# Optimization experiments

Hardware: AMD Instinct MI355X
Metric: run time of the kernel (lower is better)

Reference implementation:

```python
import jax, jax.numpy as jnp
import numpy as np

B, S, D, H = 4, 2048, 1024, 16
DK = D // H

def setup_inputs() -> dict:
    key = jax.random.key(0)
    ks = jax.random.split(key, 11)
    scale = 1.0 / np.sqrt(D)
    inp = {
        'q': jax.random.normal(ks[0], (B, S, D), jnp.float32),
        'k': jax.random.normal(ks[1], (B, S, D), jnp.float32),
        'v': jax.random.normal(ks[2], (B, S, D), jnp.float32),
        'Wq': jax.random.normal(ks[3], (D, D), jnp.float32) * scale,
        'bq': jnp.zeros((D,), jnp.float32),
        'Wk': jax.random.normal(ks[4], (D, D), jnp.float32) * scale,
        'bk': jnp.zeros((D,), jnp.float32),
        'Wv': jax.random.normal(ks[5], (D, D), jnp.float32) * scale,
        'bv': jnp.zeros((D,), jnp.float32),
        'Wo': jax.random.normal(ks[6], (D, D), jnp.float32) * scale,
        'bo': jnp.zeros((D,), jnp.float32),
        # diagonal mask: 0 on the diagonal (self position masked out), 1 elsewhere
        'mask': (1 - jnp.eye(S, dtype=jnp.int32))[None, None, :, :],
    }
    return inp


def reference(q, k, v, Wq, bq, Wk, bk, Wv, bv, Wo, bo, mask):
    def proj(x, W, b):
        # [B,S,D] -> [B,H,S,DK]
        y = x @ W.T + b
        return y.reshape(B, S, H, DK).transpose(0, 2, 1, 3)

    qh = proj(q, Wq, bq)
    kh = proj(k, Wk, bk)
    vh = proj(v, Wv, bv)

    scores = jnp.einsum('bhsd,bhtd->bhst', qh, kh) / jnp.sqrt(jnp.float32(DK))
    scores = jnp.where(mask == 0, jnp.finfo(scores.dtype).min, scores)
    attn = jax.nn.softmax(scores, axis=-1)  # dropout is identity in eval mode
    out = jnp.einsum('bhst,bhtd->bhsd', attn, vh)
    out = out.transpose(0, 2, 1, 3).reshape(B, S, D)
    return out @ Wo.T + bo
```

## Files before the change

kernel.cpp:

```cpp
#include <hip/hip_runtime.h>
#include <stdint.h>

#define S_LEN 2048
#define D_DIM 1024
#define NB 4
#define NH 16
#define DKH 64
#define M_ROWS (NB * S_LEN)
#define PLD 72

typedef float  f32x4 __attribute__((ext_vector_type(4)));
typedef short  s16x8 __attribute__((ext_vector_type(8)));
typedef unsigned short u16;
typedef u16    u16x4 __attribute__((ext_vector_type(4)));

#define AS1 __attribute__((address_space(1)))
#define AS3 __attribute__((address_space(3)))

__device__ __forceinline__ void gload16(const u16* g, u16* l) {
    __builtin_amdgcn_global_load_lds((const AS1 void*)g, (AS3 void*)l, 16, 0, 0);
}

__device__ __forceinline__ u16 f2bf(float f) {
    uint32_t u = __builtin_bit_cast(uint32_t, f);
    return (u16)((u + 0x7fffu + ((u >> 16) & 1u)) >> 16);
}
__device__ __forceinline__ u16 f2bf_cheap(float f) {
    uint32_t u = __builtin_bit_cast(uint32_t, f);
    return (u16)((u + 0x8000u) >> 16);
}

__global__ __launch_bounds__(256) void conv_kernel(const float* __restrict__ src,
                                                   u16* __restrict__ dst, int n)
{
    int i = (blockIdx.x * 256 + threadIdx.x) * 8;
    if (i + 8 > n) return;
    f32x4 a = *(const f32x4*)(src + i);
    f32x4 b = *(const f32x4*)(src + i + 4);
    s16x8 r;
#pragma unroll
    for (int j = 0; j < 4; ++j) r[j]     = (short)f2bf(a[j]);
#pragma unroll
    for (int j = 0; j < 4; ++j) r[j + 4] = (short)f2bf(b[j]);
    *(s16x8*)(dst + i) = r;
}

__global__ __launch_bounds__(256) void conv3w_kernel(const float* __restrict__ a,
                                                     const float* __restrict__ b,
                                                     const float* __restrict__ c,
                                                     u16* __restrict__ dst)
{
    const int z = blockIdx.z;
    const float* src = (z == 0) ? a : (z == 1) ? b : c;
    int i = (blockIdx.x * 256 + threadIdx.x) * 8;
    f32x4 lo = *(const f32x4*)(src + i);
    f32x4 hi = *(const f32x4*)(src + i + 4);
    s16x8 r;
#pragma unroll
    for (int j = 0; j < 4; ++j) r[j]     = (short)f2bf(lo[j]);
#pragma unroll
    for (int j = 0; j < 4; ++j) r[j + 4] = (short)f2bf(hi[j]);
    *(s16x8*)(dst + (size_t)z * (D_DIM * D_DIM) + i) = r;
}

__global__ __launch_bounds__(256) void conv3x_kernel(const float* __restrict__ a,
                                                     const float* __restrict__ b,
                                                     const float* __restrict__ c,
                                                     u16* __restrict__ da,
                                                     u16* __restrict__ db,
                                                     u16* __restrict__ dc)
{
    const int z = blockIdx.z;
    const float* src = (z == 0) ? a : (z == 1) ? b : c;
    u16* dst         = (z == 0) ? da : (z == 1) ? db : dc;
    int i = (blockIdx.x * 256 + threadIdx.x) * 8;
    f32x4 lo = *(const f32x4*)(src + i);
    f32x4 hi = *(const f32x4*)(src + i + 4);
    s16x8 r;
#pragma unroll
    for (int j = 0; j < 4; ++j) r[j]     = (short)f2bf(lo[j]);
#pragma unroll
    for (int j = 0; j < 4; ++j) r[j + 4] = (short)f2bf(hi[j]);
    *(s16x8*)(dst + i) = r;
}

__device__ __forceinline__ void stage64(const u16* __restrict__ X,
                                        const u16* __restrict__ Wt,
                                        int m0, int n0, int k0,
                                        u16* As, u16* Bs, int tid, int wv)
{
#pragma unroll
    for (int i = 0; i < 2; ++i) {
        const int c   = tid + i * 256;
        const int row = c >> 3;
        const int sg  = (c & 7) ^ (row & 7);
        gload16(&X[(size_t)(m0 + row) * D_DIM + k0 + sg * 8],
                &As[(i * 256 + wv * 64) * 8]);
    }
#pragma unroll
    for (int i = 0; i < 4; ++i) {
        const int c   = tid + i * 256;
        const int row = c >> 3;
        const int sg  = (c & 7) ^ (row & 7);
        gload16(&Wt[(size_t)(n0 + row) * D_DIM + k0 + sg * 8],
                &Bs[(i * 256 + wv * 64) * 8]);
    }
}

__device__ __forceinline__ void compute64(const u16* As, const u16* Bs,
                                          f32x4 acc[2][4],
                                          int wm, int wn, int ln, int quad, int l7)
{
#pragma unroll
    for (int ks = 0; ks < 2; ++ks) {
        const int sA = ((ks * 4 + quad) ^ l7) * 8;
        s16x8 af[2], bfr[4];
#pragma unroll
        for (int t = 0; t < 2; ++t)
            af[t]  = *(const s16x8*)&As[(wm * 32 + t * 16 + ln) * 64 + sA];
#pragma unroll
        for (int t = 0; t < 4; ++t)
            bfr[t] = *(const s16x8*)&Bs[(wn * 64 + t * 16 + ln) * 64 + sA];
#pragma unroll
        for (int tM = 0; tM < 2; ++tM)
#pragma unroll
            for (int tN = 0; tN < 4; ++tN)
                acc[tM][tN] = __builtin_amdgcn_mfma_f32_16x16x32_bf16(
                    af[tM], bfr[tN], acc[tM][tN], 0, 0, 0);
    }
}

__device__ __forceinline__ void gemm64_body(const u16* __restrict__ X,
                                            const u16* __restrict__ Wt,
                                            int m0, int n0,
                                            u16* As, u16* Bs,
                                            f32x4 acc[2][4])
{
    const int tid  = threadIdx.x;
    const int wv   = tid >> 6;
    const int lane = tid & 63;
    const int ln   = lane & 15;
    const int quad = lane >> 4;
    const int wm   = wv >> 1;
    const int wn   = wv & 1;
    const int l7   = ln & 7;

    for (int k0 = 0; k0 < D_DIM; k0 += 64) {
        __syncthreads();
        stage64(X, Wt, m0, n0, k0, As, Bs, tid, wv);
        __syncthreads();
        compute64(As, Bs, acc, wm, wn, ln, quad, l7);
    }
}

__global__ __launch_bounds__(256) void proj64_kernel(
    const u16* __restrict__ xq, const u16* __restrict__ xk,
    const u16* __restrict__ xv, const u16* __restrict__ Wb,
    const float* __restrict__ bq, const float* __restrict__ bk,
    const float* __restrict__ bv,
    u16* __restrict__ Qh, u16* __restrict__ Kh, u16* __restrict__ Vt,
    int mode0)
{
    __shared__ __attribute__((aligned(16))) u16 As[64 * 64];
    __shared__ __attribute__((aligned(16))) u16 Bs[128 * 64];

    const int mode = mode0 + blockIdx.z;
    const u16* X      = (mode == 0) ? xq : (mode == 1) ? xk : xv;
    const u16* Wt     = Wb + (size_t)mode * (D_DIM * D_DIM);
    const float* bias = (mode == 0) ? bq : (mode == 1) ? bk : bv;
    const float qscale = (mode == 0) ? 0.18033688011112042f : 1.0f;

    const int lin = blockIdx.y * 8 + blockIdx.x;
    const int n0  = (lin & 7) * 128;
    const int m0  = (lin >> 3) * 64;

    f32x4 zero = {0.f, 0.f, 0.f, 0.f};
    f32x4 acc[2][4];
#pragma unroll
    for (int i = 0; i < 2; ++i)
#pragma unroll
        for (int j = 0; j < 4; ++j) acc[i][j] = zero;

    gemm64_body(X, Wt, m0, n0, As, Bs, acc);

    const int tid  = threadIdx.x;
    const int wv   = tid >> 6;
    const int lane = tid & 63;
    const int ln   = lane & 15;
    const int quad = lane >> 4;
    const int wm   = wv >> 1;
    const int wn   = wv & 1;

#pragma unroll
    for (int tM = 0; tM < 2; ++tM) {
#pragma unroll
        for (int tN = 0; tN < 4; ++tN) {
            const int ng = n0 + wn * 64 + tN * 16 + ln;
            const float bf32 = bias[ng];
            const int h  = ng >> 6;
            const int dk = ng & 63;
            const int mbase = m0 + wm * 32 + tM * 16 + quad * 4;
            const int b = mbase >> 11;
            const int s = mbase & 2047;
            if (mode == 2) {
                u16x4 pk;
#pragma unroll
                for (int r = 0; r < 4; ++r) pk[r] = f2bf(acc[tM][tN][r] + bf32);
                *(u16x4*)&Vt[((size_t)((b * NH + h) * DKH + dk)) * S_LEN + s] = pk;
            } else {
                u16* dst = (mode == 0) ? Qh : Kh;
#pragma unroll
                for (int r = 0; r < 4; ++r)
                    dst[((size_t)(b * NH + h) * S_LEN + (s + r)) * DKH + dk] =
                        f2bf((acc[tM][tN][r] + bf32) * qscale);
            }
        }
    }
}

__global__ __launch_bounds__(256) void attn_kernel(
    const u16* __restrict__ Qh, const u16* __restrict__ Kh,
    const u16* __restrict__ Vt, u16* __restrict__ ctx)
{
    __shared__ __attribute__((aligned(16))) u16 Ks[64 * 64];
    __shared__ __attribute__((aligned(16))) u16 Vs[64 * 64];
    __shared__ __attribute__((aligned(16))) u16 QPs[64 * PLD];

    const int tid  = threadIdx.x;
    const int wv   = tid >> 6;
    const int lane = tid & 63;
    const int ln   = lane & 15;
    const int quad = lane >> 4;
    const int l7   = ln & 7;

    const int lin = blockIdx.y * 32 + blockIdx.x;
    const int xcd = lin & 7;
    const int t_  = lin >> 3;
    const int bh  = xcd * 8 + (t_ >> 5);
    const int q0  = (t_ & 31) * 64;

    const size_t qkbase = (size_t)bh * S_LEN * DKH;
    const size_t vbase  = (size_t)bh * DKH * S_LEN;

#pragma unroll
    for (int i = 0; i < 2; ++i) {
        const int c = tid + i * 256, row = c >> 3;
        const int sg = (c & 7) ^ (row & 7);
        gload16(&Qh[qkbase + (size_t)(q0 + row) * DKH + sg * 8],
                &QPs[(i * 256 + wv * 64) * 8]);
    }
    __syncthreads();

    s16x8 aq[2];
#pragma unroll
    for (int ks = 0; ks < 2; ++ks)
        aq[ks] = *(const s16x8*)&QPs[(wv * 16 + ln) * 64 + (((ks * 4 + quad) ^ l7) * 8)];

    float l_part[4] = {0.f, 0.f, 0.f, 0.f};
    f32x4 zero = {0.f, 0.f, 0.f, 0.f};
    f32x4 o_acc[4] = {zero, zero, zero, zero};

    const int rbase = q0 + wv * 16 + quad * 4;
    const int rowA = wv * 16 + ln;
    const int rotA = (((rowA >> 2) & 7)) * 8;
    const int rotW = ((4 * wv + quad) & 7) * 8;

    for (int kb = 0; kb < S_LEN; kb += 64) {
        __syncthreads();
#pragma unroll
        for (int i = 0; i < 2; ++i) {
            const int c = tid + i * 256, row = c >> 3;
            const int sg = (c & 7) ^ (row & 7);
            const int lb = (i * 256 + wv * 64) * 8;
            gload16(&Kh[qkbase + (size_t)(kb + row) * DKH + sg * 8], &Ks[lb]);
            gload16(&Vt[vbase + (size_t)row * S_LEN + kb + sg * 8], &Vs[lb]);
        }
        __syncthreads();

        f32x4 sf[4];
#pragma unroll
        for (int nt = 0; nt < 4; ++nt) {
            f32x4 acc = zero;
#pragma unroll
            for (int ks = 0; ks < 2; ++ks) {
                s16x8 bk_ = *(const s16x8*)&Ks[(nt * 16 + ln) * 64 + (((ks * 4 + quad) ^ l7) * 8)];
                acc = __builtin_amdgcn_mfma_f32_16x16x32_bf16(aq[ks], bk_, acc, 0, 0, 0);
            }
            sf[nt] = acc;
        }

        if (kb == q0) {
#pragma unroll
            for (int nt = 0; nt < 4; ++nt)
#pragma unroll
                for (int r = 0; r < 4; ++r) {
                    float p = __builtin_amdgcn_exp2f(sf[nt][r]);
                    if (rbase + r == kb + nt * 16 + ln) p = 0.f;
                    sf[nt][r] = p;
                    l_part[r] += p;
                }
        } else {
#pragma unroll
            for (int nt = 0; nt < 4; ++nt)
#pragma unroll
                for (int r = 0; r < 4; ++r) {
                    float p = __builtin_amdgcn_exp2f(sf[nt][r]);
                    sf[nt][r] = p;
                    l_part[r] += p;
                }
        }

#pragma unroll
        for (int nt = 0; nt < 4; ++nt)
#pragma unroll
            for (int r = 0; r < 4; ++r) {
                int row  = wv * 16 + quad * 4 + r;
                int col  = ((nt * 16 + ln) + rotW) & 63;
                QPs[row * PLD + col] = f2bf_cheap(sf[nt][r]);
            }

#pragma unroll
        for (int ks = 0; ks < 2; ++ks) {
            int colA = ((ks * 32 + quad * 8) + rotA) & 63;
            s16x8 ap = *(const s16x8*)&QPs[rowA * PLD + colA];
#pragma unroll
            for (int nt = 0; nt < 4; ++nt) {
                s16x8 bvv = *(const s16x8*)&Vs[(nt * 16 + ln) * 64 + (((ks * 4 + quad) ^ l7) * 8)];
                o_acc[nt] = __builtin_amdgcn_mfma_f32_16x16x32_bf16(ap, bvv, o_acc[nt], 0, 0, 0);
            }
        }
    }

#pragma unroll
    for (int r = 0; r < 4; ++r) {
#pragma unroll
        for (int off = 1; off < 16; off <<= 1)
            l_part[r] += __shfl_xor(l_part[r], off, 16);
    }

    const int b = bh >> 4;
    const int h = bh & 15;
#pragma unroll
    for (int nt = 0; nt < 4; ++nt) {
#pragma unroll
        for (int r = 0; r < 4; ++r) {
            float val = o_acc[nt][r] / l_part[r];
            int sg = q0 + wv * 16 + quad * 4 + r;
            ctx[((size_t)b * S_LEN + sg) * D_DIM + h * DKH + nt * 16 + ln] = f2bf(val);
        }
    }
}

__global__ __launch_bounds__(256) void oproj64_kernel(
    const u16* __restrict__ ctx, const u16* __restrict__ WoB,
    const float* __restrict__ bo, float* __restrict__ out, float sentinel)
{
    __shared__ __attribute__((aligned(16))) u16 As[64 * 64];
    __shared__ __attribute__((aligned(16))) u16 Bs[128 * 64];

    const int lin = blockIdx.y * 8 + blockIdx.x;
    const int n0  = (lin & 7) * 128;
    const int m0  = (lin >> 3) * 64;

    f32x4 zero = {0.f, 0.f, 0.f, 0.f};
    f32x4 acc[2][4];
#pragma unroll
    for (int i = 0; i < 2; ++i)
#pragma unroll
        for (int j = 0; j < 4; ++j) acc[i][j] = zero;

    gemm64_body(ctx, WoB, m0, n0, As, Bs, acc);

    const int tid  = threadIdx.x;
    const int wv   = tid >> 6;
    const int lane = tid & 63;
    const int ln   = lane & 15;
    const int quad = lane >> 4;
    const int wm   = wv >> 1;
    const int wn   = wv & 1;

#pragma unroll
    for (int tM = 0; tM < 2; ++tM) {
#pragma unroll
        for (int tN = 0; tN < 4; ++tN) {
            const int ng = n0 + wn * 64 + tN * 16 + ln;
            const float bf32 = bo[ng];
            const int mbase = m0 + wm * 32 + tM * 16 + quad * 4;
#pragma unroll
            for (int r = 0; r < 4; ++r) {
                float val = acc[tM][tN][r] + bf32;
                if (mbase + r == 0 && ng == 0) val += sentinel;
                out[(size_t)(mbase + r) * D_DIM + ng] = val;
            }
        }
    }
}

extern "C" void kernel_launch(void* const* d_in, const int* in_sizes, int n_in,
                              void* d_out, int out_size, void* d_ws, size_t ws_size,
                              hipStream_t stream)
{
    const float* q  = (const float*)d_in[0];
    const float* k  = (const float*)d_in[1];
    const float* v  = (const float*)d_in[2];
    const float* Wq = (const float*)d_in[3];
    const float* bq = (const float*)d_in[4];
    const float* Wk = (const float*)d_in[5];
    const float* bk = (const float*)d_in[6];
    const float* Wv = (const float*)d_in[7];
    const float* bv = (const float*)d_in[8];
    const float* Wo = (const float*)d_in[9];
    const float* bo = (const float*)d_in[10];

    const size_t headSz = (size_t)NB * NH * S_LEN * DKH;
    const int    WN     = D_DIM * D_DIM;
    u16* Qh  = (u16*)d_ws;
    u16* Kh  = Qh + headSz;
    u16* Vt  = Kh + headSz;
    u16* ctx = Vt + headSz;
    u16* Wb  = (u16*)d_out;
    u16* xk  = Wb + 3 * WN;
    u16* xv  = Qh;
    u16* xq  = ctx;
    u16* WoB = Qh;
    float* out = (float*)d_out;

    float sentinel = 0.f;
    {
        const int expect[12] = {8388608, 8388608, 8388608, 1048576, 1024, 1048576,
                                1024, 1048576, 1024, 1048576, 1024, 4194304};
        bool ok = (n_in == 12);
        for (int i = 0; ok && i < 12; ++i) ok = (in_sizes[i] == expect[i]);
        if (!ok)                               sentinel = 1000.f;
        else if (ws_size < 4 * headSz * 2)     sentinel = 2000.f;
        else if (out_size != (int)headSz)      sentinel = 3000.f;
    }

    conv3w_kernel<<<dim3(WN / 2048, 1, 3), 256, 0, stream>>>(Wq, Wk, Wv, Wb);
    conv3x_kernel<<<dim3((int)(headSz / 2048), 1, 3), 256, 0, stream>>>(
        v, q, k, xv, xq, xk);

    proj64_kernel<<<dim3(8, M_ROWS / 64, 1), 256, 0, stream>>>(
        xq, xk, xv, Wb, bq, bk, bv, Qh, Kh, Vt, 2);
    proj64_kernel<<<dim3(8, M_ROWS / 64, 2), 256, 0, stream>>>(
        xq, xk, xv, Wb, bq, bk, bv, Qh, Kh, Vt, 0);

    attn_kernel<<<dim3(32, 64), 256, 0, stream>>>(Qh, Kh, Vt, ctx);

    conv_kernel<<<dim3(WN / 2048), 256, 0, stream>>>(Wo, WoB, WN);

    oproj64_kernel<<<dim3(8, M_ROWS / 64), 256, 0, stream>>>(ctx, WoB, bo, out, sentinel);
}
```

Measured before the change: 431.3 us.

## Use 128x128 GEMM tiles, fuse V fp32 conversion, split-K output projection

Projection and output GEMMs move from 64x128 to 128x128 block tiles, with each wave computing 64x64 outputs, to raise operand reuse per LDS load. The V input is now converted from fp32 to bf16 inside the projection kernel while staging, which removes one conversion pass and merges the three projections into a single launch. The output projection is split in two along K, with the second half written to a scratch buffer and summed by a new add kernel. This trades fewer blocks, higher register use and an extra fp32 read/write pass for better tile efficiency. The fused V staging uses synchronous register loads rather than async LDS loads.

```diff
diff --git a/kernel.cpp b/kernel.cpp
--- a/kernel.cpp
+++ b/kernel.cpp
@@ -63,16 +63,13 @@
     *(s16x8*)(dst + (size_t)z * (D_DIM * D_DIM) + i) = r;
 }
 
-__global__ __launch_bounds__(256) void conv3x_kernel(const float* __restrict__ a,
-                                                     const float* __restrict__ b,
-                                                     const float* __restrict__ c,
-                                                     u16* __restrict__ da,
-                                                     u16* __restrict__ db,
-                                                     u16* __restrict__ dc)
-{
-    const int z = blockIdx.z;
-    const float* src = (z == 0) ? a : (z == 1) ? b : c;
-    u16* dst         = (z == 0) ? da : (z == 1) ? db : dc;
+__global__ __launch_bounds__(256) void conv2_kernel(const float* __restrict__ a,
+                                                    const float* __restrict__ b,
+                                                    u16* __restrict__ da,
+                                                    u16* __restrict__ db)
+{
+    const float* src = blockIdx.z ? b : a;
+    u16* dst        = blockIdx.z ? db : da;
     int i = (blockIdx.x * 256 + threadIdx.x) * 8;
     f32x4 lo = *(const f32x4*)(src + i);
     f32x4 hi = *(const f32x4*)(src + i + 4);
@@ -84,45 +81,51 @@
     *(s16x8*)(dst + i) = r;
 }
 
-__device__ __forceinline__ void stage64(const u16* __restrict__ X,
-                                        const u16* __restrict__ Wt,
-                                        int m0, int n0, int k0,
-                                        u16* As, u16* Bs, int tid, int wv)
-{
-#pragma unroll
-    for (int i = 0; i < 2; ++i) {
-        const int c   = tid + i * 256;
-        const int row = c >> 3;
-        const int sg  = (c & 7) ^ (row & 7);
-        gload16(&X[(size_t)(m0 + row) * D_DIM + k0 + sg * 8],
-                &As[(i * 256 + wv * 64) * 8]);
-    }
+__global__ __launch_bounds__(256) void add_kernel(float* __restrict__ out,
+                                                  const float* __restrict__ P)
+{
+    int i = (blockIdx.x * 256 + threadIdx.x) * 8;
+    f32x4 a = *(const f32x4*)(out + i);
+    f32x4 b = *(const f32x4*)(P + i);
+    f32x4 c = *(const f32x4*)(out + i + 4);
+    f32x4 d = *(const f32x4*)(P + i + 4);
+#pragma unroll
+    for (int j = 0; j < 4; ++j) { a[j] += b[j]; c[j] += d[j]; }
+    *(f32x4*)(out + i)     = a;
+    *(f32x4*)(out + i + 4) = c;
+}
+
+__device__ __forceinline__ void stage_tile(const u16* __restrict__ X,
+                                           const u16* __restrict__ Wt,
+                                           int m0, int n0, int k0,
+                                           u16* As, u16* Bs, int tid, int wv)
+{
 #pragma unroll
     for (int i = 0; i < 4; ++i) {
         const int c   = tid + i * 256;
         const int row = c >> 3;
         const int sg  = (c & 7) ^ (row & 7);
-        gload16(&Wt[(size_t)(n0 + row) * D_DIM + k0 + sg * 8],
-                &Bs[(i * 256 + wv * 64) * 8]);
-    }
-}
-
-__device__ __forceinline__ void compute64(const u16* As, const u16* Bs,
-                                          f32x4 acc[2][4],
-                                          int wm, int wn, int ln, int quad, int l7)
+        const int lb  = (i * 256 + wv * 64) * 8;
+        gload16(&X [(size_t)(m0 + row) * D_DIM + k0 + sg * 8], &As[lb]);
+        gload16(&Wt[(size_t)(n0 + row) * D_DIM + k0 + sg * 8], &Bs[lb]);
+    }
+}
+
+__device__ __forceinline__ void compute_tile(const u16* As, const u16* Bs,
+                                             f32x4 acc[4][4],
+                                             int wm, int wn, int ln, int quad, int l7)
 {
 #pragma unroll
     for (int ks = 0; ks < 2; ++ks) {
         const int sA = ((ks * 4 + quad) ^ l7) * 8;
-        s16x8 af[2], bfr[4];
-#pragma unroll
-        for (int t = 0; t < 2; ++t)
-            af[t]  = *(const s16x8*)&As[(wm * 32 + t * 16 + ln) * 64 + sA];
-#pragma unroll
-        for (int t = 0; t < 4; ++t)
+        s16x8 af[4], bfr[4];
+#pragma unroll
+        for (int t = 0; t < 4; ++t) {
+            af[t]  = *(const s16x8*)&As[(wm * 64 + t * 16 + ln) * 64 + sA];
             bfr[t] = *(const s16x8*)&Bs[(wn * 64 + t * 16 + ln) * 64 + sA];
-#pragma unroll
-        for (int tM = 0; tM < 2; ++tM)
+        }
+#pragma unroll
+        for (int tM = 0; tM < 4; ++tM)
 #pragma unroll
             for (int tN = 0; tN < 4; ++tN)
                 acc[tM][tN] = __builtin_amdgcn_mfma_f32_16x16x32_bf16(
@@ -130,11 +133,11 @@
     }
 }
 
-__device__ __forceinline__ void gemm64_body(const u16* __restrict__ X,
-                                            const u16* __restrict__ Wt,
-                                            int m0, int n0,
-                                            u16* As, u16* Bs,
-                                            f32x4 acc[2][4])
+__device__ __forceinline__ void gemm128_body(const u16* __restrict__ X,
+                                             const u16* __restrict__ Wt,
+                                             int m0, int n0, int kbeg, int kend,
+                                             u16* As, u16* Bs,
+                                             f32x4 acc[4][4])
 {
     const int tid  = threadIdx.x;
     const int wv   = tid >> 6;
@@ -145,43 +148,32 @@
     const int wn   = wv & 1;
     const int l7   = ln & 7;
 
-    for (int k0 = 0; k0 < D_DIM; k0 += 64) {
-        __syncthreads();
-        stage64(X, Wt, m0, n0, k0, As, Bs, tid, wv);
-        __syncthreads();
-        compute64(As, Bs, acc, wm, wn, ln, quad, l7);
-    }
-}
-
-__global__ __launch_bounds__(256) void proj64_kernel(
+    for (int k0 = kbeg; k0 < kend; k0 += 64) {
+        __syncthreads();
+        stage_tile(X, Wt, m0, n0, k0, As, Bs, tid, wv);
+        __syncthreads();
+        compute_tile(As, Bs, acc, wm, wn, ln, quad, l7);
+    }
+}
+
+__global__ __launch_bounds__(256, 4) void proj_kernel(
     const u16* __restrict__ xq, const u16* __restrict__ xk,
-    const u16* __restrict__ xv, const u16* __restrict__ Wb,
+    const float* __restrict__ vf, const u16* __restrict__ Wb,
     const float* __restrict__ bq, const float* __restrict__ bk,
     const float* __restrict__ bv,
-    u16* __restrict__ Qh, u16* __restrict__ Kh, u16* __restrict__ Vt,
-    int mode0)
-{
-    __shared__ __attribute__((aligned(16))) u16 As[64 * 64];
+    u16* __restrict__ Qh, u16* __restrict__ Kh, u16* __restrict__ Vt)
+{
+    __shared__ __attribute__((aligned(16))) u16 As[128 * 64];
     __shared__ __attribute__((aligned(16))) u16 Bs[128 * 64];
 
-    const int mode = mode0 + blockIdx.z;
-    const u16* X      = (mode == 0) ? xq : (mode == 1) ? xk : xv;
+    const int mode = blockIdx.z;
+    const u16* X      = (mode == 0) ? xq : xk;
     const u16* Wt     = Wb + (size_t)mode * (D_DIM * D_DIM);
     const float* bias = (mode == 0) ? bq : (mode == 1) ? bk : bv;
     const float qscale = (mode == 0) ? 0.18033688011112042f : 1.0f;
 
-    const int lin = blockIdx.y * 8 + blockIdx.x;
-    const int n0  = (lin & 7) * 128;
-    const int m0  = (lin >> 3) * 64;
-
-    f32x4 zero = {0.f, 0.f, 0.f, 0.f};
-    f32x4 acc[2][4];
-#pragma unroll
-    for (int i = 0; i < 2; ++i)
-#pragma unroll
-        for (int j = 0; j < 4; ++j) acc[i][j] = zero;
-
-    gemm64_body(X, Wt, m0, n0, As, Bs, acc);
+    const int n0 = blockIdx.x * 128;
+    const int m0 = blockIdx.y * 128;
 
     const int tid  = threadIdx.x;
     const int wv   = tid >> 6;
@@ -190,16 +182,57 @@
     const int quad = lane >> 4;
     const int wm   = wv >> 1;
     const int wn   = wv & 1;
-
-#pragma unroll
-    for (int tM = 0; tM < 2; ++tM) {
+    const int l7   = ln & 7;
+
+    f32x4 zero = {0.f, 0.f, 0.f, 0.f};
+    f32x4 acc[4][4];
+#pragma unroll
+    for (int i = 0; i < 4; ++i)
+#pragma unroll
+        for (int j = 0; j < 4; ++j) acc[i][j] = zero;
+
+    for (int k0 = 0; k0 < D_DIM; k0 += 64) {
+        __syncthreads();
+        if (mode == 2) {
+#pragma unroll
+            for (int c = 0; c < 4; ++c) {
+                const int slot = tid + c * 256;
+                const int row  = slot >> 3;
+                const int sl   = slot & 7;
+                const float* s = vf + (size_t)(m0 + row) * D_DIM + k0 + sl * 8;
+                f32x4 lo = *(const f32x4*)s;
+                f32x4 hi = *(const f32x4*)(s + 4);
+                s16x8 r;
+#pragma unroll
+                for (int j = 0; j < 4; ++j) r[j]     = (short)f2bf(lo[j]);
+#pragma unroll
+                for (int j = 0; j < 4; ++j) r[j + 4] = (short)f2bf(hi[j]);
+                *(s16x8*)&As[row * 64 + ((sl ^ (row & 7)) * 8)] = r;
+            }
+#pragma unroll
+            for (int i = 0; i < 4; ++i) {
+                const int c   = tid + i * 256;
+                const int row = c >> 3;
+                const int sg  = (c & 7) ^ (row & 7);
+                gload16(&Wt[(size_t)(n0 + row) * D_DIM + k0 + sg * 8],
+                        &Bs[(i * 256 + wv * 64) * 8]);
+            }
+        } else {
+            stage_tile(X, Wt, m0, n0, k0, As, Bs, tid, wv);
+        }
+        __syncthreads();
+        compute_tile(As, Bs, acc, wm, wn, ln, quad, l7);
+    }
+
+#pragma unroll
+    for (int tM = 0; tM < 4; ++tM) {
 #pragma unroll
         for (int tN = 0; tN < 4; ++tN) {
             const int ng = n0 + wn * 64 + tN * 16 + ln;
             const float bf32 = bias[ng];
             const int h  = ng >> 6;
             const int dk = ng & 63;
-            const int mbase = m0 + wm * 32 + tM * 16 + quad * 4;
+            const int mbase = m0 + wm * 64 + tM * 16 + quad * 4;
             const int b = mbase >> 11;
             const int s = mbase & 2047;
             if (mode == 2) {
@@ -351,25 +384,26 @@
     }
 }
 
-__global__ __launch_bounds__(256) void oproj64_kernel(
+__global__ __launch_bounds__(256, 4) void oproj_kernel(
     const u16* __restrict__ ctx, const u16* __restrict__ WoB,
-    const float* __restrict__ bo, float* __restrict__ out, float sentinel)
-{
-    __shared__ __attribute__((aligned(16))) u16 As[64 * 64];
+    const float* __restrict__ bo, float* __restrict__ out,
+    float* __restrict__ P, float sentinel)
+{
+    __shared__ __attribute__((aligned(16))) u16 As[128 * 64];
     __shared__ __attribute__((aligned(16))) u16 Bs[128 * 64];
 
-    const int lin = blockIdx.y * 8 + blockIdx.x;
-    const int n0  = (lin & 7) * 128;
-    const int m0  = (lin >> 3) * 64;
+    const int kz = blockIdx.z;
+    const int n0 = blockIdx.x * 128;
+    const int m0 = blockIdx.y * 128;
 
     f32x4 zero = {0.f, 0.f, 0.f, 0.f};
-    f32x4 acc[2][4];
-#pragma unroll
-    for (int i = 0; i < 2; ++i)
+    f32x4 acc[4][4];
+#pragma unroll
+    for (int i = 0; i < 4; ++i)
 #pragma unroll
         for (int j = 0; j < 4; ++j) acc[i][j] = zero;
 
-    gemm64_body(ctx, WoB, m0, n0, As, Bs, acc);
+    gemm128_body(ctx, WoB, m0, n0, kz * 512, kz * 512 + 512, As, Bs, acc);
 
     const int tid  = threadIdx.x;
     const int wv   = tid >> 6;
@@ -380,17 +414,23 @@
     const int wn   = wv & 1;
 
 #pragma unroll
-    for (int tM = 0; tM < 2; ++tM) {
+    for (int tM = 0; tM < 4; ++tM) {
 #pragma unroll
         for (int tN = 0; tN < 4; ++tN) {
             const int ng = n0 + wn * 64 + tN * 16 + ln;
-            const float bf32 = bo[ng];
-            const int mbase = m0 + wm * 32 + tM * 16 + quad * 4;
-#pragma unroll
-            for (int r = 0; r < 4; ++r) {
-                float val = acc[tM][tN][r] + bf32;
-                if (mbase + r == 0 && ng == 0) val += sentinel;
-                out[(size_t)(mbase + r) * D_DIM + ng] = val;
+            const int mbase = m0 + wm * 64 + tM * 16 + quad * 4;
+            if (kz == 0) {
+                const float bf32 = bo[ng];
+#pragma unroll
+                for (int r = 0; r < 4; ++r) {
+                    float val = acc[tM][tN][r] + bf32;
+                    if (mbase + r == 0 && ng == 0) val += sentinel;
+                    out[(size_t)(mbase + r) * D_DIM + ng] = val;
+                }
+            } else {
+#pragma unroll
+                for (int r = 0; r < 4; ++r)
+                    P[(size_t)(mbase + r) * D_DIM + ng] = acc[tM][tN][r];
             }
         }
     }
@@ -420,9 +460,9 @@
     u16* ctx = Vt + headSz;
     u16* Wb  = (u16*)d_out;
     u16* xk  = Wb + 3 * WN;
-    u16* xv  = Qh;
     u16* xq  = ctx;
     u16* WoB = Qh;
+    float* P = (float*)Kh;
     float* out = (float*)d_out;
 
     float sentinel = 0.f;
@@ -437,17 +477,16 @@
     }
 
     conv3w_kernel<<<dim3(WN / 2048, 1, 3), 256, 0, stream>>>(Wq, Wk, Wv, Wb);
-    conv3x_kernel<<<dim3((int)(headSz / 2048), 1, 3), 256, 0, stream>>>(
-        v, q, k, xv, xq, xk);
-
-    proj64_kernel<<<dim3(8, M_ROWS / 64, 1), 256, 0, stream>>>(
-        xq, xk, xv, Wb, bq, bk, bv, Qh, Kh, Vt, 2);
-    proj64_kernel<<<dim3(8, M_ROWS / 64, 2), 256, 0, stream>>>(
-        xq, xk, xv, Wb, bq, bk, bv, Qh, Kh, Vt, 0);
+    conv2_kernel<<<dim3((int)(headSz / 2048), 1, 2), 256, 0, stream>>>(q, k, xq, xk);
+
+    proj_kernel<<<dim3(8, M_ROWS / 128, 3), 256, 0, stream>>>(
+        xq, xk, v, Wb, bq, bk, bv, Qh, Kh, Vt);
 
     attn_kernel<<<dim3(32, 64), 256, 0, stream>>>(Qh, Kh, Vt, ctx);
 
     conv_kernel<<<dim3(WN / 2048), 256, 0, stream>>>(Wo, WoB, WN);
 
-    oproj64_kernel<<<dim3(8, M_ROWS / 64), 256, 0, stream>>>(ctx, WoB, bo, out, sentinel);
-}
+    oproj_kernel<<<dim3(8, M_ROWS / 128, 2), 256, 0, stream>>>(
+        ctx, WoB, bo, out, P, sentinel);
+    add_kernel<<<dim3((int)(M_ROWS * (size_t)D_DIM / 2048)), 256, 0, stream>>>(out, P);
+}
```

Result: faster. 419.4 us (-2.7%).
